# Performance work log

Hardware: AMD Instinct MI355X
Metric: run time of the kernel (lower is better)

Reference implementation:

```python
import jax, jax.numpy as jnp
import numpy as np

N_NODES = 50000
N_EDGES = 1000000
IN_DIM, HID_DIM, OUT_DIM = 128, 64, 16


def setup_inputs() -> dict:
    key = jax.random.key(0)
    k1, k2, k3, k4 = jax.random.split(key, 4)
    x = jax.random.normal(k1, (N_NODES, IN_DIM), dtype=jnp.float32)
    edge_index = jax.random.randint(k2, (2, N_EDGES), 0, N_NODES, dtype=jnp.int64)
    # Glorot-style scaling for weights, zero bias (PyG GCNConv default init style)
    W1 = jax.random.normal(k3, (IN_DIM, HID_DIM), dtype=jnp.float32) * (1.0 / np.sqrt(IN_DIM))
    b1 = jnp.zeros((HID_DIM,), dtype=jnp.float32)
    W2 = jax.random.normal(k4, (HID_DIM, OUT_DIM), dtype=jnp.float32) * (1.0 / np.sqrt(HID_DIM))
    b2 = jnp.zeros((OUT_DIM,), dtype=jnp.float32)
    return {"x": x, "edge_index": edge_index, "W1": W1, "b1": b1, "W2": W2, "b2": b2}


def gcn_conv(x, src, dst, W, b, num_nodes):
    """PyG GCNConv: add self loops, symmetric deg^{-1/2} normalization,
    linear transform, gather-scale-scatter aggregation, bias."""
    # degree includes self loops (src/dst already augmented by caller)
    deg = jax.ops.segment_sum(jnp.ones_like(dst, dtype=x.dtype), dst, num_segments=num_nodes)
    dinv = jnp.where(deg > 0, deg ** -0.5, 0.0)
    norm = dinv[src] * dinv[dst]            # [E']
    h = x @ W                                # [N, F_out] transform before aggregation
    msg = h[src] * norm[:, None]             # gather + scale
    out = jax.ops.segment_sum(msg, dst, num_segments=num_nodes)  # scatter-add
    return out + b


def reference(x, edge_index, W1, b1, W2, b2):
    n = x.shape[0]
    loops = jnp.arange(n, dtype=edge_index.dtype)
    src = jnp.concatenate([edge_index[0], loops])
    dst = jnp.concatenate([edge_index[1], loops])
    h = gcn_conv(x, src, dst, W1, b1, n)
    h = jax.nn.relu(h)
    out = gcn_conv(h, src, dst, W2, b2, n)
    return out
```

## Files before the change

kernel.cpp:

```cpp
#include <hip/hip_runtime.h>

#define IN_DIM 128
#define HID_DIM 64
#define OUT_DIM 16

#define SSHIFT 7
#define SMASK 127
#define CHUNK 4096
#define CBLK 1024
#define KPT (CHUNK / CBLK)
#define CAP 4096

#define G1N 64
#define G1S 132

static __device__ __forceinline__ unsigned short f2bf(float f) {
    unsigned u = __float_as_uint(f);
    unsigned r = u + 0x7fffu + ((u >> 16) & 1u);
    return (unsigned short)(r >> 16);
}
static __device__ __forceinline__ unsigned packbf2(float a, float b) {
    return (unsigned)f2bf(a) | ((unsigned)f2bf(b) << 16);
}
static __device__ __forceinline__ float bflo(unsigned v) { return __uint_as_float(v << 16); }
static __device__ __forceinline__ float bfhi(unsigned v) { return __uint_as_float(v & 0xffff0000u); }

__global__ __launch_bounds__(CBLK) void passC2(const int* __restrict__ src,
                                               const int* __restrict__ dst,
                                               int* __restrict__ gcnt,
                                               int* __restrict__ eb,
                                               int E, int NS) {
    __shared__ int cnt[512];
    __shared__ int lofs[512];
    __shared__ int bofs[512];
    __shared__ int cur[512];
    __shared__ int srt[CHUNK];
    int t = threadIdx.x;
    if (t < 512) cnt[t] = 0;
    __syncthreads();
    int base = blockIdx.x * CHUNK;
    int dreg[KPT];
    #pragma unroll
    for (int k = 0; k < KPT; ++k) {
        int i = base + k * CBLK + t;
        int d = -1;
        if (i < E) { d = dst[i]; atomicAdd(&cnt[d >> SSHIFT], 1); }
        dreg[k] = d;
    }
    __syncthreads();
    if (t < 512) lofs[t] = cnt[t];
    __syncthreads();
    for (int off = 1; off < 512; off <<= 1) {
        int tmp = 0;
        if (t < 512 && t >= off) tmp = lofs[t - off];
        __syncthreads();
        if (t < 512) lofs[t] += tmp;
        __syncthreads();
    }
    if (t < 512) {
        int c  = cnt[t];
        int lo = lofs[t] - c;
        lofs[t] = lo;
        cur[t]  = lo;
        bofs[t] = (t < NS && c) ? atomicAdd(&gcnt[t], c) : 0;
    }
    __syncthreads();
    #pragma unroll
    for (int k = 0; k < KPT; ++k) {
        int i = base + k * CBLK + t;
        if (i < E) {
            int d = dreg[k];
            int s = d >> SSHIFT;
            int p = atomicAdd(&cur[s], 1);
            srt[p] = src[i] | ((d & SMASK) << 17);
        }
    }
    __syncthreads();
    int wave = t >> 6, lane = t & 63;
    for (int s = wave; s < NS; s += CBLK / 64) {
        int c  = cnt[s];
        int lo = lofs[s];
        size_t gb = (size_t)s * CAP + bofs[s];
        for (int k = lane; k < c; k += 64) eb[gb + k] = srt[lo + k];
    }
}

__global__ __launch_bounds__(256) void passD(const int* __restrict__ eb,
                                             const int* __restrict__ tot,
                                             int* __restrict__ csr_src,
                                             int* __restrict__ row_ptr,
                                             float* __restrict__ dinv,
                                             int N, int E, int NS) {
    __shared__ int red[256];
    __shared__ int deg[128], incl[128], cur[128];
    __shared__ int srt[CAP];
    int s = blockIdx.x, t = threadIdx.x;
    if (t < 128) deg[t] = 0;
    int part = 0;
    for (int k = t; k < s; k += 256) part += tot[k];
    red[t] = part;
    __syncthreads();
    for (int off = 128; off >= 1; off >>= 1) {
        if (t < off) red[t] += red[t + off];
        __syncthreads();
    }
    int b0 = red[0];
    int cnt = tot[s];
    const size_t sbase = (size_t)s * CAP;
    for (int k = t; k < cnt; k += 256) atomicAdd(&deg[eb[sbase + k] >> 17], 1);
    __syncthreads();
    if (t < 128) incl[t] = deg[t];
    __syncthreads();
    for (int off = 1; off < 128; off <<= 1) {
        int tmp = 0;
        if (t < 128 && t >= off) tmp = incl[t - off];
        __syncthreads();
        if (t < 128) incl[t] += tmp;
        __syncthreads();
    }
    if (t < 128) {
        int loff = incl[t] - deg[t];
        cur[t] = loff;
        int n = (s << SSHIFT) + t;
        if (n < N) {
            row_ptr[n] = b0 + loff;
            dinv[n] = rsqrtf((float)(deg[t] + 1));
        }
    }
    if (s == NS - 1 && t == 0) row_ptr[N] = E;
    __syncthreads();
    for (int k = t; k < cnt; k += 256) {
        int v = eb[sbase + k];
        int dl = v >> 17;
        int p = atomicAdd(&cur[dl], 1);
        srt[p] = v & 0x1FFFF;
    }
    __syncthreads();
    for (int k = t; k < cnt; k += 256) csr_src[b0 + k] = srt[k];
}

__global__ __launch_bounds__(256) void gemm1_kernel(const float* __restrict__ x,
                                                    const float* __restrict__ W1,
                                                    const float* __restrict__ dinv,
                                                    unsigned* __restrict__ h1u, int N) {
    __shared__ __align__(16) float sW[IN_DIM * HID_DIM];
    __shared__ __align__(16) float sx[G1N * G1S];
    int t = threadIdx.x;
    int node0 = blockIdx.x * G1N;

    const float4* W4  = (const float4*)W1;
    float4*       sW4 = (float4*)sW;
    #pragma unroll
    for (int i = 0; i < 8; ++i) sW4[i * 256 + t] = W4[i * 256 + t];

    const float4* x4 = (const float4*)x;
    for (int i = t; i < G1N * 32; i += 256) {
        int r = i >> 5, c = i & 31;
        int n = node0 + r; if (n >= N) n = 0;
        *(float4*)(sx + r * G1S + c * 4) = x4[(size_t)n * 32 + c];
    }
    __syncthreads();

    int og = t & 15, ng = t >> 4;
    float a00=0.f,a01=0.f,a02=0.f,a03=0.f, a10=0.f,a11=0.f,a12=0.f,a13=0.f,
          a20=0.f,a21=0.f,a22=0.f,a23=0.f, a30=0.f,a31=0.f,a32=0.f,a33=0.f;
    const float* xr = sx + (ng << 2) * G1S;
    #pragma unroll 4
    for (int k = 0; k < IN_DIM; ++k) {
        float x0 = xr[k];
        float x1 = xr[G1S + k];
        float x2 = xr[2 * G1S + k];
        float x3 = xr[3 * G1S + k];
        float4 wv = ((const float4*)(sW + k * HID_DIM))[og];
        a00 = fmaf(x0, wv.x, a00); a01 = fmaf(x0, wv.y, a01);
        a02 = fmaf(x0, wv.z, a02); a03 = fmaf(x0, wv.w, a03);
        a10 = fmaf(x1, wv.x, a10); a11 = fmaf(x1, wv.y, a11);
        a12 = fmaf(x1, wv.z, a12); a13 = fmaf(x1, wv.w, a13);
        a20 = fmaf(x2, wv.x, a20); a21 = fmaf(x2, wv.y, a21);
        a22 = fmaf(x2, wv.z, a22); a23 = fmaf(x2, wv.w, a23);
        a30 = fmaf(x3, wv.x, a30); a31 = fmaf(x3, wv.y, a31);
        a32 = fmaf(x3, wv.z, a32); a33 = fmaf(x3, wv.w, a33);
    }

    int nb = node0 + (ng << 2);
#define G1_STORE(i, c0, c1, c2, c3)                                         \
    {                                                                       \
        int n = nb + i;                                                     \
        if (n <= N) {                                                       \
            float dn = (n < N) ? dinv[n] : 0.f;         \
            uint2 pv;                                                       \
            pv.x = packbf2(c0 * dn, c1 * dn);                               \
            pv.y = packbf2(c2 * dn, c3 * dn);                               \
            ((uint2*)(h1u + (size_t)n * 32))[og] = pv;                      \
        }                                                                   \
    }
    G1_STORE(0, a00, a01, a02, a03)
    G1_STORE(1, a10, a11, a12, a13)
    G1_STORE(2, a20, a21, a22, a23)
    G1_STORE(3, a30, a31, a32, a33)
#undef G1_STORE
}

__global__ __launch_bounds__(256) void agg1_kernel(const unsigned* __restrict__ h1u,
                                                   const int* __restrict__ row_ptr,
                                                   const int* __restrict__ csr_src,
                                                   const float* __restrict__ dinv,
                                                   const float* __restrict__ b1,
                                                   const float* __restrict__ W2,
                                                   unsigned* __restrict__ h2u, int N) {
    __shared__ __align__(16) float sW[OUT_DIM * 68];
    int t = threadIdx.x;
    for (int i = t; i < HID_DIM * OUT_DIM; i += 256) {
        int k = i >> 4, j = i & 15;
        sW[j * 68 + k] = W2[i];
    }
    __syncthreads();

    int lane = t & 63;
    int h  = lane >> 5;
    int l  = lane & 31;
    int es = l >> 3;
    int dg = l & 7;
    int n = blockIdx.x * 8 + ((t >> 6) << 1) + h;
    if (n > N) return;
    if (n == N) {
        if (l < 4) { uint2 z; z.x = 0u; z.y = 0u; ((uint2*)h2u)[(size_t)N * 4 + l] = z; }
        return;
    }

    int e0 = row_ptr[n], e1 = row_ptr[n + 1];
    const uint4* rb = (const uint4*)h1u;
    int sb = h << 5;

    float a0 = 0.f, a1 = 0.f, a2 = 0.f, a3 = 0.f,
          a4 = 0.f, a5 = 0.f, a6 = 0.f, a7 = 0.f;

    for (int base = e0 - 1; base < e1; base += 32) {
        int idx = base + l;
        int sld = N;
        if (idx == e0 - 1) sld = n;
        else if (idx < e1) sld = csr_src[idx];
        int lim = e1 - base;
        if (lim > 32) lim = 32;
        int nr = (lim + 3) >> 2;
        nr = (nr + 1) & ~1;
        for (int r = 0; r < nr; r += 2) {
            int sA = __shfl(sld, sb + ((r + 0) << 2) + es);
            int sB = __shfl(sld, sb + ((r + 1) << 2) + es);
            uint4 vA = rb[(size_t)sA * 8 + dg];
            uint4 vB = rb[(size_t)sB * 8 + dg];
            a0 += bflo(vA.x) + bflo(vB.x);
            a1 += bfhi(vA.x) + bfhi(vB.x);
            a2 += bflo(vA.y) + bflo(vB.y);
            a3 += bfhi(vA.y) + bfhi(vB.y);
            a4 += bflo(vA.z) + bflo(vB.z);
            a5 += bfhi(vA.z) + bfhi(vB.z);
            a6 += bflo(vA.w) + bflo(vB.w);
            a7 += bfhi(vA.w) + bfhi(vB.w);
        }
    }
    #pragma unroll
    for (int m = 8; m <= 16; m <<= 1) {
        a0 += __shfl_xor(a0, m); a1 += __shfl_xor(a1, m);
        a2 += __shfl_xor(a2, m); a3 += __shfl_xor(a3, m);
        a4 += __shfl_xor(a4, m); a5 += __shfl_xor(a5, m);
        a6 += __shfl_xor(a6, m); a7 += __shfl_xor(a7, m);
    }

    float dn = dinv[n];
    float4 bA = ((const float4*)b1)[2 * dg];
    float4 bB = ((const float4*)b1)[2 * dg + 1];
    float r0 = fmaxf(fmaf(dn, a0, bA.x), 0.f);
    float r1 = fmaxf(fmaf(dn, a1, bA.y), 0.f);
    float r2 = fmaxf(fmaf(dn, a2, bA.z), 0.f);
    float r3 = fmaxf(fmaf(dn, a3, bA.w), 0.f);
    float r4 = fmaxf(fmaf(dn, a4, bB.x), 0.f);
    float r5 = fmaxf(fmaf(dn, a5, bB.y), 0.f);
    float r6 = fmaxf(fmaf(dn, a6, bB.z), 0.f);
    float r7 = fmaxf(fmaf(dn, a7, bB.w), 0.f);

    const float* wb = sW + ((es << 2) * 68) + (dg << 3);
    float4 wA, wB2;
    wA = *(const float4*)(wb);        wB2 = *(const float4*)(wb + 4);
    float p0 = r0*wA.x + r1*wA.y + r2*wA.z + r3*wA.w + r4*wB2.x + r5*wB2.y + r6*wB2.z + r7*wB2.w;
    wA = *(const float4*)(wb + 68);   wB2 = *(const float4*)(wb + 72);
    float p1 = r0*wA.x + r1*wA.y + r2*wA.z + r3*wA.w + r4*wB2.x + r5*wB2.y + r6*wB2.z + r7*wB2.w;
    wA = *(const float4*)(wb + 136);  wB2 = *(const float4*)(wb + 140);
    float p2 = r0*wA.x + r1*wA.y + r2*wA.z + r3*wA.w + r4*wB2.x + r5*wB2.y + r6*wB2.z + r7*wB2.w;
    wA = *(const float4*)(wb + 204);  wB2 = *(const float4*)(wb + 208);
    float p3 = r0*wA.x + r1*wA.y + r2*wA.z + r3*wA.w + r4*wB2.x + r5*wB2.y + r6*wB2.z + r7*wB2.w;

    #pragma unroll
    for (int m = 1; m <= 4; m <<= 1) {
        p0 += __shfl_xor(p0, m); p1 += __shfl_xor(p1, m);
        p2 += __shfl_xor(p2, m); p3 += __shfl_xor(p3, m);
    }
    if (dg == 0) {
        uint2 pv;
        pv.x = packbf2(p0 * dn, p1 * dn);
        pv.y = packbf2(p2 * dn, p3 * dn);
        ((uint2*)h2u)[(size_t)n * 4 + es] = pv;
    }
}

__global__ __launch_bounds__(256) void agg2_kernel(const unsigned* __restrict__ h2u,
                                                   const int* __restrict__ row_ptr,
                                                   const int* __restrict__ csr_src,
                                                   const float* __restrict__ dinv,
                                                   const float* __restrict__ b2,
                                                   float* __restrict__ out, int N) {
    int t = threadIdx.x;
    int lane = t & 63;
    int h  = lane >> 4;
    int l  = lane & 15;
    int es = l >> 2;
    int dg = l & 3;
    int n = blockIdx.x * 16 + ((t >> 6) << 2) + h;
    if (n >= N) return;

    int e0 = row_ptr[n], e1 = row_ptr[n + 1];
    const uint2* rb = (const uint2*)h2u;
    int sb = h << 4;

    float a0 = 0.f, a1 = 0.f, a2 = 0.f, a3 = 0.f;

    for (int base = e0 - 1; base < e1; base += 16) {
        int idx = base + l;
        int sld = N;
        if (idx == e0 - 1) sld = n;
        else if (idx < e1) sld = csr_src[idx];
        int lim = e1 - base;
        if (lim > 16) lim = 16;
        int nr = (lim + 3) >> 2;
        nr = (nr + 1) & ~1;
        for (int r = 0; r < nr; r += 2) {
            int sA = __shfl(sld, sb + ((r + 0) << 2) + es);
            int sB = __shfl(sld, sb + ((r + 1) << 2) + es);
            uint2 vA = rb[(size_t)sA * 4 + dg];
            uint2 vB = rb[(size_t)sB * 4 + dg];
            a0 += bflo(vA.x) + bflo(vB.x);
            a1 += bfhi(vA.x) + bfhi(vB.x);
            a2 += bflo(vA.y) + bflo(vB.y);
            a3 += bfhi(vA.y) + bfhi(vB.y);
        }
    }
    #pragma unroll
    for (int m = 4; m <= 8; m <<= 1) {
        a0 += __shfl_xor(a0, m); a1 += __shfl_xor(a1, m);
        a2 += __shfl_xor(a2, m); a3 += __shfl_xor(a3, m);
    }
    if (es == 0) {
        float dn = dinv[n];
        float4 bb = ((const float4*)b2)[dg];
        float4 r;
        r.x = fmaf(dn, a0, bb.x);
        r.y = fmaf(dn, a1, bb.y);
        r.z = fmaf(dn, a2, bb.z);
        r.w = fmaf(dn, a3, bb.w);
        ((float4*)out)[(size_t)n * 4 + dg] = r;
    }
}

extern "C" void kernel_launch(void* const* d_in, const int* in_sizes, int n_in,
                              void* d_out, int out_size, void* d_ws, size_t ws_size,
                              hipStream_t stream) {
    const float* x  = (const float*)d_in[0];
    const int*   ei = (const int*)d_in[1];
    const float* W1 = (const float*)d_in[2];
    const float* b1 = (const float*)d_in[3];
    const float* W2 = (const float*)d_in[4];
    const float* b2 = (const float*)d_in[5];
    float* out = (float*)d_out;

    const int N = in_sizes[0] / IN_DIM;
    const int E = in_sizes[1] / 2;
    const int* src = ei;
    const int* dst = ei + E;

    const int NS  = (N + SMASK) >> SSHIFT;
    const int NSP = NS + 1;
    const int BC  = (E + CHUNK - 1) / CHUNK;

    char* w = (char*)d_ws;
    auto alloc = [&](size_t bytes) -> void* {
        void* p = (void*)w;
        w += (bytes + 255) & ~(size_t)255;
        return p;
    };
    int*      gcnt    = (int*)     alloc((size_t)NSP * 4);
    int*      eb      = (int*)     alloc((size_t)NS * CAP * 4);
    int*      csr_src = (int*)     alloc((size_t)E * 4);
    int*      row_ptr = (int*)     alloc((size_t)(N + 1) * 4);
    float*    dinv    = (float*)   alloc((size_t)N * 4);
    unsigned* h1u     = (unsigned*)alloc((size_t)(N + 1) * 32 * 4);
    unsigned* h2u     = (unsigned*)alloc((size_t)(N + 1) * 8 * 4);

    const int GB  = (N + G1N) / G1N;
    const int AB1 = (N + 8) / 8;
    const int AB2 = (N + 15) / 16;

    hipMemsetAsync(gcnt, 0, (size_t)NSP * 4, stream);
    passC2<<<BC, CBLK, 0, stream>>>(src, dst, gcnt, eb, E, NS);
    passD <<<NS, 256,  0, stream>>>(eb, gcnt, csr_src, row_ptr, dinv, N, E, NS);

    gemm1_kernel<<<GB, 256, 0, stream>>>(x, W1, dinv, h1u, N);
    agg1_kernel<<<AB1, 256, 0, stream>>>(h1u, row_ptr, csr_src, dinv, b1, W2, h2u, N);
    agg2_kernel<<<AB2, 256, 0, stream>>>(h2u, row_ptr, csr_src, dinv, b2, out, N);
}
```

Measured before the change: 159.0 us.

## Fuse CSR finalize pass with first-layer GEMM into one kernel

Merges the per-bucket CSR build and degree normalization kernel with the x@W1 transform. Each block builds its 128-node CSR slice, keeps dinv in shared memory, then computes the scaled bf16 h1 rows for the same 128 nodes in two 64-node subtiles. This removes one kernel launch and the global dinv reload, but it cuts the GEMM grid in half and raises shared memory per block to about 67KB, which reduces occupancy and parallelism.

```diff
diff --git a/kernel.cpp b/kernel.cpp
--- a/kernel.cpp
+++ b/kernel.cpp
@@ -11,8 +11,12 @@
 #define KPT (CHUNK / CBLK)
 #define CAP 4096
 
-#define G1N 64
 #define G1S 132
+
+#define SW_OFF   0
+#define SX_OFF   32768
+#define SDV_OFF  66560
+#define SMEM_BYTES 67072
 
 static __device__ __forceinline__ unsigned short f2bf(float f) {
     unsigned u = __float_as_uint(f);
@@ -85,120 +89,141 @@
     }
 }
 
-__global__ __launch_bounds__(256) void passD(const int* __restrict__ eb,
-                                             const int* __restrict__ tot,
-                                             int* __restrict__ csr_src,
-                                             int* __restrict__ row_ptr,
-                                             float* __restrict__ dinv,
-                                             int N, int E, int NS) {
-    __shared__ int red[256];
-    __shared__ int deg[128], incl[128], cur[128];
-    __shared__ int srt[CAP];
+__global__ __launch_bounds__(256) void passDG(const int* __restrict__ eb,
+                                              const int* __restrict__ tot,
+                                              const float* __restrict__ x,
+                                              const float* __restrict__ W1,
+                                              int* __restrict__ csr_src,
+                                              int* __restrict__ row_ptr,
+                                              float* __restrict__ dinv,
+                                              unsigned* __restrict__ h1u,
+                                              int N, int E, int NS) {
+    __shared__ __align__(16) char smem[SMEM_BYTES];
     int s = blockIdx.x, t = threadIdx.x;
-    if (t < 128) deg[t] = 0;
-    int part = 0;
-    for (int k = t; k < s; k += 256) part += tot[k];
-    red[t] = part;
-    __syncthreads();
-    for (int off = 128; off >= 1; off >>= 1) {
-        if (t < off) red[t] += red[t + off];
-        __syncthreads();
-    }
-    int b0 = red[0];
-    int cnt = tot[s];
-    const size_t sbase = (size_t)s * CAP;
-    for (int k = t; k < cnt; k += 256) atomicAdd(&deg[eb[sbase + k] >> 17], 1);
-    __syncthreads();
-    if (t < 128) incl[t] = deg[t];
-    __syncthreads();
-    for (int off = 1; off < 128; off <<= 1) {
-        int tmp = 0;
-        if (t < 128 && t >= off) tmp = incl[t - off];
-        __syncthreads();
-        if (t < 128) incl[t] += tmp;
-        __syncthreads();
-    }
-    if (t < 128) {
-        int loff = incl[t] - deg[t];
-        cur[t] = loff;
-        int n = (s << SSHIFT) + t;
-        if (n < N) {
-            row_ptr[n] = b0 + loff;
-            dinv[n] = rsqrtf((float)(deg[t] + 1));
-        }
-    }
-    if (s == NS - 1 && t == 0) row_ptr[N] = E;
-    __syncthreads();
-    for (int k = t; k < cnt; k += 256) {
-        int v = eb[sbase + k];
-        int dl = v >> 17;
-        int p = atomicAdd(&cur[dl], 1);
-        srt[p] = v & 0x1FFFF;
-    }
-    __syncthreads();
-    for (int k = t; k < cnt; k += 256) csr_src[b0 + k] = srt[k];
-}
-
-__global__ __launch_bounds__(256) void gemm1_kernel(const float* __restrict__ x,
-                                                    const float* __restrict__ W1,
-                                                    const float* __restrict__ dinv,
-                                                    unsigned* __restrict__ h1u, int N) {
-    __shared__ __align__(16) float sW[IN_DIM * HID_DIM];
-    __shared__ __align__(16) float sx[G1N * G1S];
-    int t = threadIdx.x;
-    int node0 = blockIdx.x * G1N;
-
-    const float4* W4  = (const float4*)W1;
-    float4*       sW4 = (float4*)sW;
-    #pragma unroll
-    for (int i = 0; i < 8; ++i) sW4[i * 256 + t] = W4[i * 256 + t];
-
-    const float4* x4 = (const float4*)x;
-    for (int i = t; i < G1N * 32; i += 256) {
-        int r = i >> 5, c = i & 31;
-        int n = node0 + r; if (n >= N) n = 0;
-        *(float4*)(sx + r * G1S + c * 4) = x4[(size_t)n * 32 + c];
-    }
-    __syncthreads();
-
-    int og = t & 15, ng = t >> 4;
-    float a00=0.f,a01=0.f,a02=0.f,a03=0.f, a10=0.f,a11=0.f,a12=0.f,a13=0.f,
-          a20=0.f,a21=0.f,a22=0.f,a23=0.f, a30=0.f,a31=0.f,a32=0.f,a33=0.f;
-    const float* xr = sx + (ng << 2) * G1S;
-    #pragma unroll 4
-    for (int k = 0; k < IN_DIM; ++k) {
-        float x0 = xr[k];
-        float x1 = xr[G1S + k];
-        float x2 = xr[2 * G1S + k];
-        float x3 = xr[3 * G1S + k];
-        float4 wv = ((const float4*)(sW + k * HID_DIM))[og];
-        a00 = fmaf(x0, wv.x, a00); a01 = fmaf(x0, wv.y, a01);
-        a02 = fmaf(x0, wv.z, a02); a03 = fmaf(x0, wv.w, a03);
-        a10 = fmaf(x1, wv.x, a10); a11 = fmaf(x1, wv.y, a11);
-        a12 = fmaf(x1, wv.z, a12); a13 = fmaf(x1, wv.w, a13);
-        a20 = fmaf(x2, wv.x, a20); a21 = fmaf(x2, wv.y, a21);
-        a22 = fmaf(x2, wv.z, a22); a23 = fmaf(x2, wv.w, a23);
-        a30 = fmaf(x3, wv.x, a30); a31 = fmaf(x3, wv.y, a31);
-        a32 = fmaf(x3, wv.z, a32); a33 = fmaf(x3, wv.w, a33);
-    }
-
-    int nb = node0 + (ng << 2);
+
+    {
+        int* red  = (int*)smem;
+        int* deg  = red + 256;
+        int* incl = deg + 128;
+        int* cur  = incl + 128;
+        int* srt  = cur + 128;
+        float* sdv = (float*)(smem + SDV_OFF);
+
+        if (t < 128) deg[t] = 0;
+        int part = 0;
+        for (int k = t; k < s; k += 256) part += tot[k];
+        red[t] = part;
+        __syncthreads();
+        for (int off = 128; off >= 1; off >>= 1) {
+            if (t < off) red[t] += red[t + off];
+            __syncthreads();
+        }
+        int b0 = red[0];
+        int cnt = tot[s];
+        const size_t sbase = (size_t)s * CAP;
+        for (int k = t; k < cnt; k += 256) atomicAdd(&deg[eb[sbase + k] >> 17], 1);
+        __syncthreads();
+        if (t < 128) incl[t] = deg[t];
+        __syncthreads();
+        for (int off = 1; off < 128; off <<= 1) {
+            int tmp = 0;
+            if (t < 128 && t >= off) tmp = incl[t - off];
+            __syncthreads();
+            if (t < 128) incl[t] += tmp;
+            __syncthreads();
+        }
+        if (t < 128) {
+            int loff = incl[t] - deg[t];
+            cur[t] = loff;
+            float dn = rsqrtf((float)(deg[t] + 1));
+            sdv[t] = dn;
+            int n = (s << SSHIFT) + t;
+            if (n < N) {
+                row_ptr[n] = b0 + loff;
+                dinv[n] = dn;
+            }
+        }
+        if (s == NS - 1 && t == 0) row_ptr[N] = E;
+        __syncthreads();
+        for (int k = t; k < cnt; k += 256) {
+            int v = eb[sbase + k];
+            int dl = v >> 17;
+            int p = atomicAdd(&cur[dl], 1);
+            srt[p] = v & 0x1FFFF;
+        }
+        __syncthreads();
+        for (int k = t; k < cnt; k += 256) csr_src[b0 + k] = srt[k];
+    }
+    __syncthreads();
+
+    {
+        float* sW  = (float*)(smem + SW_OFF);
+        float* sx  = (float*)(smem + SX_OFF);
+        float* sdv = (float*)(smem + SDV_OFF);
+
+        const float4* W4  = (const float4*)W1;
+        float4*       sW4 = (float4*)sW;
+        #pragma unroll
+        for (int i = 0; i < 8; ++i) sW4[i * 256 + t] = W4[i * 256 + t];
+
+        const float4* x4 = (const float4*)x;
+        int og = t & 15, ng = t >> 4;
+
+        for (int st = 0; st < 2; ++st) {
+            int node0 = (s << SSHIFT) + st * 64;
+            __syncthreads();
+            for (int i = t; i < 64 * 32; i += 256) {
+                int r = i >> 5, c = i & 31;
+                int n = node0 + r; if (n >= N) n = 0;
+                *(float4*)(sx + r * G1S + c * 4) = x4[(size_t)n * 32 + c];
+            }
+            __syncthreads();
+
+            float a00=0.f,a01=0.f,a02=0.f,a03=0.f, a10=0.f,a11=0.f,a12=0.f,a13=0.f,
+                  a20=0.f,a21=0.f,a22=0.f,a23=0.f, a30=0.f,a31=0.f,a32=0.f,a33=0.f;
+            const float* xr = sx + (ng << 2) * G1S;
+            #pragma unroll 4
+            for (int k = 0; k < IN_DIM; ++k) {
+                float x0 = xr[k];
+                float x1 = xr[G1S + k];
+                float x2 = xr[2 * G1S + k];
+                float x3 = xr[3 * G1S + k];
+                float4 wv = ((const float4*)(sW + k * HID_DIM))[og];
+                a00 = fmaf(x0, wv.x, a00); a01 = fmaf(x0, wv.y, a01);
+                a02 = fmaf(x0, wv.z, a02); a03 = fmaf(x0, wv.w, a03);
+                a10 = fmaf(x1, wv.x, a10); a11 = fmaf(x1, wv.y, a11);
+                a12 = fmaf(x1, wv.z, a12); a13 = fmaf(x1, wv.w, a13);
+                a20 = fmaf(x2, wv.x, a20); a21 = fmaf(x2, wv.y, a21);
+                a22 = fmaf(x2, wv.z, a22); a23 = fmaf(x2, wv.w, a23);
+                a30 = fmaf(x3, wv.x, a30); a31 = fmaf(x3, wv.y, a31);
+                a32 = fmaf(x3, wv.z, a32); a33 = fmaf(x3, wv.w, a33);
+            }
+
+            int lb = st * 64 + (ng << 2);
+            int nb = (s << SSHIFT) + st * 64 + (ng << 2);
 #define G1_STORE(i, c0, c1, c2, c3)                                         \
-    {                                                                       \
-        int n = nb + i;                                                     \
-        if (n <= N) {                                                       \
-            float dn = (n < N) ? dinv[n] : 0.f;         \
-            uint2 pv;                                                       \
-            pv.x = packbf2(c0 * dn, c1 * dn);                               \
-            pv.y = packbf2(c2 * dn, c3 * dn);                               \
-            ((uint2*)(h1u + (size_t)n * 32))[og] = pv;                      \
-        }                                                                   \
-    }
-    G1_STORE(0, a00, a01, a02, a03)
-    G1_STORE(1, a10, a11, a12, a13)
-    G1_STORE(2, a20, a21, a22, a23)
-    G1_STORE(3, a30, a31, a32, a33)
+            {                                                               \
+                int n = nb + i;                                             \
+                if (n < N) {                                                \
+                    float dn = sdv[lb + i];                                 \
+                    uint2 pv;                                               \
+                    pv.x = packbf2(c0 * dn, c1 * dn);                       \
+                    pv.y = packbf2(c2 * dn, c3 * dn);                       \
+                    ((uint2*)(h1u + (size_t)n * 32))[og] = pv;              \
+                }                                                           \
+            }
+            G1_STORE(0, a00, a01, a02, a03)
+            G1_STORE(1, a10, a11, a12, a13)
+            G1_STORE(2, a20, a21, a22, a23)
+            G1_STORE(3, a30, a31, a32, a33)
 #undef G1_STORE
+        }
+
+        if (s == NS - 1 && t < 16) {
+            uint2 z; z.x = 0u; z.y = 0u;
+            ((uint2*)(h1u + (size_t)N * 32))[t] = z;
+        }
+    }
 }
 
 __global__ __launch_bounds__(256) void agg1_kernel(const unsigned* __restrict__ h1u,
@@ -395,15 +420,12 @@
     unsigned* h1u     = (unsigned*)alloc((size_t)(N + 1) * 32 * 4);
     unsigned* h2u     = (unsigned*)alloc((size_t)(N + 1) * 8 * 4);
 
-    const int GB  = (N + G1N) / G1N;
     const int AB1 = (N + 8) / 8;
     const int AB2 = (N + 15) / 16;
 
     hipMemsetAsync(gcnt, 0, (size_t)NSP * 4, stream);
     passC2<<<BC, CBLK, 0, stream>>>(src, dst, gcnt, eb, E, NS);
-    passD <<<NS, 256,  0, stream>>>(eb, gcnt, csr_src, row_ptr, dinv, N, E, NS);
-
-    gemm1_kernel<<<GB, 256, 0, stream>>>(x, W1, dinv, h1u, N);
+    passDG<<<NS, 256, 0, stream>>>(eb, gcnt, x, W1, csr_src, row_ptr, dinv, h1u, N, E, NS);
     agg1_kernel<<<AB1, 256, 0, stream>>>(h1u, row_ptr, csr_src, dinv, b1, W2, h2u, N);
     agg2_kernel<<<AB2, 256, 0, stream>>>(h2u, row_ptr, csr_src, dinv, b2, out, N);
 }
```

New measurement: 156.0 us (median of 2 runs). No clear change (-1.9%).
